# Performance work log

Hardware: AMD Instinct MI355X
Metric: run time of the kernel (lower is better)

## Reference

```python
import jax, jax.numpy as jnp
import numpy as np

B, M, K, E, V, HOPS = 256, 128, 4, 512, 32000, 3


def setup_inputs() -> dict:
    key = jax.random.key(0)
    ks = jax.random.split(key, 12)

    def emb_table(k):
        t = 0.1 * jax.random.normal(k, (V, E), dtype=jnp.float32)
        return t.at[0].set(0.0)  # padding_idx=0

    inp = {
        "context": jax.random.randint(ks[0], (B, M, K), 0, V),
        "y_": jax.random.randint(ks[1], (B,), 0, V),
        "h_": jax.random.normal(ks[2], (1, B, E), dtype=jnp.float32),
        # embedding tables; C[i] tied to A[i+1], so distinct: A0,A1,A2,C2
        "A0": emb_table(ks[3]),
        "A1": emb_table(ks[4]),
        "A2": emb_table(ks[5]),
        "C2": emb_table(ks[6]),
        # GRU (single layer, single step): PyTorch layout [3E, E] and [3E]
        "W_ih": 0.05 * jax.random.normal(ks[7], (3 * E, E), dtype=jnp.float32),
        "W_hh": 0.05 * jax.random.normal(ks[8], (3 * E, E), dtype=jnp.float32),
        "b_ih": jnp.zeros((3 * E,), dtype=jnp.float32),
        "b_hh": jnp.zeros((3 * E,), dtype=jnp.float32),
        # lin_vocab: Linear(2E -> V)
        "lin_W": 0.02 * jax.random.normal(ks[9], (V, 2 * E), dtype=jnp.float32),
        "lin_b": jnp.zeros((V,), dtype=jnp.float32),
    }
    return inp


def _gru_step(x, h, W_ih, W_hh, b_ih, b_hh):
    gi = x @ W_ih.T + b_ih  # [B, 3E]
    gh = h @ W_hh.T + b_hh
    i_r, i_z, i_n = jnp.split(gi, 3, axis=-1)
    h_r, h_z, h_n = jnp.split(gh, 3, axis=-1)
    r = jax.nn.sigmoid(i_r + h_r)
    z = jax.nn.sigmoid(i_z + h_z)
    n = jnp.tanh(i_n + r * h_n)
    return (1.0 - z) * n + z * h


def reference(context, y_, h_, A0, A1, A2, C2, W_ih, W_hh, b_ih, b_hh, lin_W, lin_b):
    # memories[hop] = sum_k A[hop][context], memories[hops] = sum_k C[hops-1][context]
    tables = [A0, A1, A2, C2]
    memories = [t[context].sum(axis=2) for t in tables]  # each [B, M, E]

    m = A1[y_]  # C[0](y_) -- C[0].weight tied to A[1].weight, [B, E]
    h = _gru_step(m, h_[0], W_ih, W_hh, b_ih, b_hh)  # [B, E]

    q = h
    p = None
    p_vocab = None
    for hop in range(HOPS):
        p = jnp.einsum("bme,be->bm", memories[hop], q)  # dot-attention scores
        attn = jax.nn.softmax(p, axis=1)
        o = jnp.einsum("bm,bme->be", attn, memories[hop + 1])
        if hop == 0:
            p_vocab = jnp.concatenate([q, o], axis=1) @ lin_W.T + lin_b  # [B, V]
        q = q + o

    p_ptr = p  # last hop's pre-softmax scores [B, M]
    return (p_ptr, p_vocab, h[None])  # h: [1, B, E]
```

## Files before the change

### kernel.cpp

```cpp
#include <hip/hip_runtime.h>
#include <hip/hip_bf16.h>
#include <stdint.h>
#include <stddef.h>

#define Bb 256
#define Mm 128
#define Ee 512
#define Vv 32000
#define E3 1536

typedef __attribute__((ext_vector_type(8))) short bf16x8;
typedef __attribute__((ext_vector_type(4))) float f32x4;

__device__ __forceinline__ float bf2f(unsigned short u) {
  union { unsigned int i; float f; } v; v.i = ((unsigned int)u) << 16; return v.f;
}
__device__ __forceinline__ unsigned int f2bf(float f) {
  union { float f; unsigned int u; } v; v.f = f;
  unsigned int u = v.u;
  return ((u + 0x7fffu + ((u >> 16) & 1u)) >> 16);
}

#define IN2F_IDX(bb, col)                                                     \
  ((((size_t)((bb) >> 4) * 32 + ((col) >> 5)) * 512) +                        \
   (size_t)((((bb) & 15) + (((col) >> 3) & 3) * 16) * 8 + ((col) & 7)))

__global__ void convert_kernel(const float* __restrict__ A0, const float* __restrict__ A1,
                               const float* __restrict__ A2,
                               unsigned short* __restrict__ tabB) {
  const int t = blockIdx.y;
  const float* src = (t == 0) ? A0 : (t == 1) ? A1 : A2;
  unsigned short* dst = tabB + (size_t)t * Vv * Ee;
  const int n4 = Vv * Ee / 4;
  for (int i = blockIdx.x * blockDim.x + threadIdx.x; i < n4; i += gridDim.x * blockDim.x) {
    f32x4 v = __builtin_nontemporal_load((const f32x4*)src + i);
    unsigned int o0 = f2bf(v.x) | (f2bf(v.y) << 16);
    unsigned int o1 = f2bf(v.z) | (f2bf(v.w) << 16);
    ((uint2*)dst)[i] = make_uint2(o0, o1);
  }
}

__global__ void gru_gemm_kernel(const int* __restrict__ y,
                                const float* __restrict__ A1,
                                const float* __restrict__ hprev,
                                const float* __restrict__ W_ih,
                                const float* __restrict__ W_hh,
                                float* __restrict__ gi,
                                float* __restrict__ gh) {
  const int z = blockIdx.z;
  const float* W = z ? W_hh : W_ih;
  float* C = z ? gh : gi;
  const int by = blockIdx.x * 64;
  const int jy = blockIdx.y * 64;
  __shared__ float As[16][65];
  __shared__ float Bs[16][65];
  const int tx = threadIdx.x & 15, ty = threadIdx.x >> 4;
  float acc[4][4] = {};
  for (int k0 = 0; k0 < Ee; k0 += 16) {
#pragma unroll
    for (int it = 0; it < 4; ++it) {
      int r = ty + it * 16;
      int row = by + r;
      const float* arow = z ? (hprev + (size_t)row * Ee) : (A1 + (size_t)y[row] * Ee);
      As[tx][r] = arow[k0 + tx];
      Bs[tx][r] = W[(size_t)(jy + r) * Ee + k0 + tx];
    }
    __syncthreads();
#pragma unroll
    for (int kk = 0; kk < 16; ++kk) {
      float a[4], bb[4];
#pragma unroll
      for (int i = 0; i < 4; ++i) { a[i] = As[kk][ty * 4 + i]; bb[i] = Bs[kk][tx * 4 + i]; }
#pragma unroll
      for (int i = 0; i < 4; ++i)
#pragma unroll
        for (int j = 0; j < 4; ++j)
          acc[i][j] += a[i] * bb[j];
    }
    __syncthreads();
  }
#pragma unroll
  for (int i = 0; i < 4; ++i)
#pragma unroll
    for (int j = 0; j < 4; ++j)
      C[(size_t)(by + ty * 4 + i) * E3 + jy + tx * 4 + j] = acc[i][j];
}

__global__ __launch_bounds__(1024) void fused_kernel(
    const int* __restrict__ ctx,
    const unsigned short* __restrict__ tabB,
    const float* __restrict__ A0, const float* __restrict__ A1,
    const float* __restrict__ A2,
    const float* __restrict__ gi, const float* __restrict__ gh,
    const float* __restrict__ b_ih, const float* __restrict__ b_hh,
    const float* __restrict__ h0,
    float* __restrict__ out_h, unsigned short* __restrict__ in2f,
    float* __restrict__ p_out) {
  extern __shared__ char smem[];
  unsigned short* Vlds = (unsigned short*)smem;
  float* p_lds = (float*)(smem + 131072);
  float* qbuf = (float*)(smem + 131584);
  float* obuf = (float*)(smem + 133632);

  const int b = blockIdx.x;
  const int tid = threadIdx.x;
  const int lane = tid & 63, w = tid >> 6;

  if (tid < 512) {
    const int e = tid;
    const float* gib = gi + (size_t)b * E3;
    const float* ghb = gh + (size_t)b * E3;
    float ir = gib[e] + b_ih[e];
    float iz = gib[512 + e] + b_ih[512 + e];
    float inn = gib[1024 + e] + b_ih[1024 + e];
    float hr = ghb[e] + b_hh[e];
    float hz = ghb[512 + e] + b_hh[512 + e];
    float hn = ghb[1024 + e] + b_hh[1024 + e];
    float r = 1.f / (1.f + __expf(-(ir + hr)));
    float z = 1.f / (1.f + __expf(-(iz + hz)));
    float n = tanhf(inn + r * hn);
    float hp = h0[(size_t)b * Ee + e];
    float hnew = (1.f - z) * n + z * hp;
    out_h[(size_t)b * Ee + e] = hnew;
    in2f[IN2F_IDX(b, e)] = (unsigned short)f2bf(hnew);
    qbuf[e] = hnew;
  }

#define GATHER_B(T)                                                          \
  {                                                                          \
    const unsigned short* Tb = tabB + (size_t)(T) * ((size_t)Vv * Ee);       \
    _Pragma("unroll 2")                                                      \
    for (int r8 = 0; r8 < 8; ++r8) {                                         \
      const int row = w * 8 + r8;                                            \
      const int4 cc = *(const int4*)(ctx + ((size_t)b * Mm + row) * 4);      \
      uint4 va = *(const uint4*)(Tb + (size_t)cc.x * Ee + lane * 8);         \
      uint4 vb = *(const uint4*)(Tb + (size_t)cc.y * Ee + lane * 8);         \
      uint4 vc = *(const uint4*)(Tb + (size_t)cc.z * Ee + lane * 8);         \
      uint4 vd = *(const uint4*)(Tb + (size_t)cc.w * Ee + lane * 8);         \
      const unsigned int* pa = (const unsigned int*)&va;                     \
      const unsigned int* pb = (const unsigned int*)&vb;                     \
      const unsigned int* pc = (const unsigned int*)&vc;                     \
      const unsigned int* pd = (const unsigned int*)&vd;                     \
      unsigned int o[4];                                                     \
      _Pragma("unroll")                                                      \
      for (int j = 0; j < 4; ++j) {                                          \
        float lo = bf2f((unsigned short)(pa[j] & 0xffff)) +                  \
                   bf2f((unsigned short)(pb[j] & 0xffff)) +                  \
                   bf2f((unsigned short)(pc[j] & 0xffff)) +                  \
                   bf2f((unsigned short)(pd[j] & 0xffff));                   \
        float hi = bf2f((unsigned short)(pa[j] >> 16)) +                     \
                   bf2f((unsigned short)(pb[j] >> 16)) +                     \
                   bf2f((unsigned short)(pc[j] >> 16)) +                     \
                   bf2f((unsigned short)(pd[j] >> 16));                      \
        o[j] = f2bf(lo) | (f2bf(hi) << 16);                                  \
      }                                                                      \
      *(uint4*)(Vlds + (size_t)row * Ee + lane * 8) = *(uint4*)o;            \
    }                                                                        \
  }

#define GATHER_F(TAB)                                                        \
  {                                                                          \
    _Pragma("unroll 2")                                                      \
    for (int r8 = 0; r8 < 8; ++r8) {                                         \
      const int row = w * 8 + r8;                                            \
      const int4 cc = *(const int4*)(ctx + ((size_t)b * Mm + row) * 4);      \
      const float* s0 = TAB + (size_t)cc.x * Ee + lane * 8;                  \
      const float* s1 = TAB + (size_t)cc.y * Ee + lane * 8;                  \
      const float* s2 = TAB + (size_t)cc.z * Ee + lane * 8;                  \
      const float* s3 = TAB + (size_t)cc.w * Ee + lane * 8;                  \
      float4 a0 = *(const float4*)s0, a1 = *(const float4*)(s0 + 4);         \
      float4 b0 = *(const float4*)s1, b1 = *(const float4*)(s1 + 4);         \
      float4 c0 = *(const float4*)s2, c1 = *(const float4*)(s2 + 4);         \
      float4 d0 = *(const float4*)s3, d1 = *(const float4*)(s3 + 4);         \
      unsigned int o[4];                                                     \
      o[0] = f2bf(a0.x + b0.x + c0.x + d0.x) |                               \
             (f2bf(a0.y + b0.y + c0.y + d0.y) << 16);                        \
      o[1] = f2bf(a0.z + b0.z + c0.z + d0.z) |                               \
             (f2bf(a0.w + b0.w + c0.w + d0.w) << 16);                        \
      o[2] = f2bf(a1.x + b1.x + c1.x + d1.x) |                               \
             (f2bf(a1.y + b1.y + c1.y + d1.y) << 16);                        \
      o[3] = f2bf(a1.z + b1.z + c1.z + d1.z) |                               \
             (f2bf(a1.w + b1.w + c1.w + d1.w) << 16);                        \
      *(uint4*)(Vlds + (size_t)row * Ee + lane * 8) = *(uint4*)o;            \
    }                                                                        \
  }

#define GATHER(T, TAB) { if (tabB) GATHER_B(T) else GATHER_F(TAB) }

#define SCORE_PHASE(EMIT)                                                    \
  {                                                                          \
    float qf[8];                                                             \
    *(float4*)&qf[0] = *(const float4*)&qbuf[lane * 8];                      \
    *(float4*)&qf[4] = *(const float4*)&qbuf[lane * 8 + 4];                  \
    _Pragma("unroll")                                                        \
    for (int r = 0; r < 8; ++r) {                                            \
      const int m = w * 8 + r;                                               \
      uint4 kv = *(const uint4*)(Vlds + (size_t)m * Ee + lane * 8);          \
      const unsigned int* p4 = (const unsigned int*)&kv;                     \
      float s = 0.f;                                                         \
      _Pragma("unroll")                                                      \
      for (int x = 0; x < 4; ++x) {                                          \
        s += bf2f((unsigned short)(p4[x] & 0xffff)) * qf[2 * x];             \
        s += bf2f((unsigned short)(p4[x] >> 16)) * qf[2 * x + 1];            \
      }                                                                      \
      _Pragma("unroll")                                                      \
      for (int off = 32; off > 0; off >>= 1) s += __shfl_down(s, off);       \
      if (lane == 0) { EMIT; }                                               \
    }                                                                        \
  }

#define SOFTMAX_PHASE                                                        \
  if (tid < 64) {                                                            \
    float v0 = p_lds[tid], v1 = p_lds[tid + 64];                             \
    float mx = fmaxf(v0, v1);                                                \
    _Pragma("unroll")                                                        \
    for (int off = 32; off > 0; off >>= 1) mx = fmaxf(mx, __shfl_xor(mx, off)); \
    float e0 = __expf(v0 - mx), e1 = __expf(v1 - mx);                        \
    float s = e0 + e1;                                                       \
    _Pragma("unroll")                                                        \
    for (int off = 32; off > 0; off >>= 1) s += __shfl_xor(s, off);          \
    float inv = 1.f / s;                                                     \
    p_lds[tid] = e0 * inv;                                                   \
    p_lds[tid + 64] = e1 * inv;                                              \
  }

#define O_PHASE                                                              \
  {                                                                          \
    const int g = tid >> 8, t = tid & 255;                                   \
    const int e2 = t * 2;                                                    \
    float a0 = 0.f, a1 = 0.f;                                                \
    _Pragma("unroll 4")                                                      \
    for (int m = g * 32; m < g * 32 + 32; ++m) {                             \
      unsigned int vv = *(const unsigned int*)(Vlds + (size_t)m * Ee + e2);  \
      float ww = p_lds[m];                                                   \
      a0 += ww * bf2f((unsigned short)(vv & 0xffff));                        \
      a1 += ww * bf2f((unsigned short)(vv >> 16));                           \
    }                                                                        \
    obuf[g * 512 + e2] = a0;                                                 \
    obuf[g * 512 + e2 + 1] = a1;                                             \
  }

  GATHER(0, A0)
  __syncthreads();
  SCORE_PHASE(p_lds[m] = s)
  __syncthreads();
  SOFTMAX_PHASE
  GATHER(1, A1)
  __syncthreads();
  O_PHASE
  __syncthreads();
  if (tid < 512) {
    const int e = tid;
    float o = obuf[e] + obuf[512 + e] + obuf[1024 + e] + obuf[1536 + e];
    qbuf[e] = qbuf[e] + o;
    in2f[IN2F_IDX(b, 512 + e)] = (unsigned short)f2bf(o);
  }
  __syncthreads();

  SCORE_PHASE(p_lds[m] = s)
  __syncthreads();
  SOFTMAX_PHASE
  GATHER(2, A2)
  __syncthreads();
  O_PHASE
  __syncthreads();
  if (tid < 512) {
    const int e = tid;
    qbuf[e] = qbuf[e] + obuf[e] + obuf[512 + e] + obuf[1024 + e] + obuf[1536 + e];
  }
  __syncthreads();

  SCORE_PHASE(p_out[b * Mm + m] = s)
}

__global__ __launch_bounds__(512) void pvocab_kernel(
    const unsigned short* __restrict__ in2f,
    const float* __restrict__ lin_W,
    const float* __restrict__ lin_b,
    float* __restrict__ out_pv) {
  const int v0 = blockIdx.x * 64;
  const int tid = threadIdx.x;
  const int lane = tid & 63, w = tid >> 6;
  const int wm = w >> 2, wn = w & 3;
  const int l15 = lane & 15, lg = lane >> 4;
  __shared__ __align__(16) unsigned short Ws[2][64][64];

  const int wc = tid & 15, wrb = tid >> 4;

  f32x4 acc[8];
#pragma unroll
  for (int i = 0; i < 8; ++i) acc[i] = (f32x4){0.f, 0.f, 0.f, 0.f};

  float4 wR[2];

#define PV_STAGE_LOAD(K0)                                                    \
  {                                                                          \
    _Pragma("unroll")                                                        \
    for (int it = 0; it < 2; ++it) {                                         \
      int r = wrb + it * 32;                                                 \
      wR[it] = *(const float4*)(lin_W + (size_t)(v0 + r) * 1024 + (K0) + wc * 4); \
    }                                                                        \
  }

#define PV_STAGE_WRITE(BUF)                                                  \
  {                                                                          \
    _Pragma("unroll")                                                        \
    for (int it = 0; it < 2; ++it) {                                         \
      int r = wrb + it * 32;                                                 \
      unsigned int o0 = f2bf(wR[it].x) | (f2bf(wR[it].y) << 16);             \
      unsigned int o1 = f2bf(wR[it].z) | (f2bf(wR[it].w) << 16);             \
      int u = wc >> 1, h = wc & 1;                                           \
      *(uint2*)(&Ws[BUF][r][((u + r) & 7) * 8 + h * 4]) = make_uint2(o0, o1); \
    }                                                                        \
  }

  PV_STAGE_LOAD(0)
  PV_STAGE_WRITE(0)
  __syncthreads();

  int cur = 0;
  for (int t = 0; t < 16; ++t) {
    if (t + 1 < 16) PV_STAGE_LOAD((t + 1) * 64)
#pragma unroll
    for (int kk = 0; kk < 2; ++kk) {
      const int cu = kk * 4 + lg;
      const int kb = t * 2 + kk;
      bf16x8 wf, af[8];
      {
        int row = wn * 16 + l15;
        wf = *(const bf16x8*)(&Ws[cur][row][((cu + row) & 7) * 8]);
      }
#pragma unroll
      for (int i = 0; i < 8; ++i) {
        int mblk = wm * 8 + i;
        af[i] = *(const bf16x8*)(in2f + ((size_t)(mblk * 32 + kb)) * 512 + lane * 8);
      }
#pragma unroll
      for (int i = 0; i < 8; ++i)
        acc[i] = __builtin_amdgcn_mfma_f32_16x16x32_bf16(af[i], wf, acc[i], 0, 0, 0);
    }
    if (t + 1 < 16) {
      PV_STAGE_WRITE(cur ^ 1)
      __syncthreads();
      cur ^= 1;
    }
  }

  {
    int v = v0 + wn * 16 + l15;
    float bias = lin_b[v];
#pragma unroll
    for (int i = 0; i < 8; ++i) {
      int brow = wm * 128 + i * 16 + lg * 4;
#pragma unroll
      for (int rr = 0; rr < 4; ++rr)
        out_pv[(size_t)(brow + rr) * Vv + v] = acc[i][rr] + bias;
    }
  }
}

extern "C" void kernel_launch(void* const* d_in, const int* in_sizes, int n_in,
                              void* d_out, int out_size, void* d_ws, size_t ws_size,
                              hipStream_t stream) {
  const int* ctx = (const int*)d_in[0];
  const int* y = (const int*)d_in[1];
  const float* h0 = (const float*)d_in[2];
  const float* A0 = (const float*)d_in[3];
  const float* A1 = (const float*)d_in[4];
  const float* A2 = (const float*)d_in[5];
  const float* W_ih = (const float*)d_in[7];
  const float* W_hh = (const float*)d_in[8];
  const float* b_ih = (const float*)d_in[9];
  const float* b_hh = (const float*)d_in[10];
  const float* lin_W = (const float*)d_in[11];
  const float* lin_b = (const float*)d_in[12];

  const size_t tabBytes = (size_t)3 * Vv * Ee * 2;
  const size_t giBytes = (size_t)Bb * E3 * 4;
  const size_t in2Bytes = (size_t)Bb * 1024 * 2;
  const bool bf16path = ws_size >= tabBytes + 2 * giBytes + in2Bytes;

  char* ws = (char*)d_ws;
  size_t off = 0;
  unsigned short* tabB = nullptr;
  if (bf16path) { tabB = (unsigned short*)ws; off += tabBytes; }
  float* gi = (float*)(ws + off); off += giBytes;
  float* gh = (float*)(ws + off); off += giBytes;
  unsigned short* in2f = (unsigned short*)(ws + off);

  float* out = (float*)d_out;
  float* p_ptr = out;
  float* p_voc = out + Bb * Mm;
  float* out_h = out + Bb * Mm + (size_t)Bb * Vv;

  if (bf16path)
    convert_kernel<<<dim3(4096, 3), 256, 0, stream>>>(A0, A1, A2, tabB);
  gru_gemm_kernel<<<dim3(4, 24, 2), 256, 0, stream>>>(y, A1, h0, W_ih, W_hh, gi, gh);
  hipFuncSetAttribute((const void*)fused_kernel,
                      hipFuncAttributeMaxDynamicSharedMemorySize, 141824);
  fused_kernel<<<Bb, 1024, 141824, stream>>>(ctx, tabB, A0, A1, A2, gi, gh,
                                             b_ih, b_hh, h0, out_h, in2f, p_ptr);
  pvocab_kernel<<<Vv / 64, 512, 0, stream>>>(in2f, lin_W, lin_b, p_voc);
}
```

Before: 228.7 us.

## Remap pvocab warp tiling and double-buffer A fragments in registers

The p_vocab GEMM kernel changes its per-warp tile from 8 M-blocks × 1 N-fragment to 2 M-blocks × 4 N-fragments. Each warp now loads far fewer A fragments from global memory per k-step and reuses each W fragment from LDS across 2 MFMAs. A fragments are prefetched two iterations ahead into alternating register buffers, and the loop is fully unrolled. The barrier is replaced by an explicit lgkmcnt wait plus s_barrier, and launch bounds request 2 blocks per SM. The costs are higher register pressure and added scheduling complexity.

```diff
diff --git a/kernel.cpp b/kernel.cpp
--- a/kernel.cpp
+++ b/kernel.cpp
@@ -273,36 +273,47 @@
   SCORE_PHASE(p_out[b * Mm + m] = s)
 }
 
-__global__ __launch_bounds__(512) void pvocab_kernel(
+__global__ __launch_bounds__(512, 2) void pvocab_kernel(
     const unsigned short* __restrict__ in2f,
     const float* __restrict__ lin_W,
     const float* __restrict__ lin_b,
     float* __restrict__ out_pv) {
+  __shared__ __align__(16) unsigned short Ws[2][64][64];
+
   const int v0 = blockIdx.x * 64;
   const int tid = threadIdx.x;
   const int lane = tid & 63, w = tid >> 6;
-  const int wm = w >> 2, wn = w & 3;
   const int l15 = lane & 15, lg = lane >> 4;
-  __shared__ __align__(16) unsigned short Ws[2][64][64];
-
   const int wc = tid & 15, wrb = tid >> 4;
 
-  f32x4 acc[8];
-#pragma unroll
-  for (int i = 0; i < 8; ++i) acc[i] = (f32x4){0.f, 0.f, 0.f, 0.f};
-
+  f32x4 acc[2][4];
+#pragma unroll
+  for (int i = 0; i < 2; ++i)
+#pragma unroll
+    for (int j = 0; j < 4; ++j)
+      acc[i][j] = (f32x4){0.f, 0.f, 0.f, 0.f};
+
+  uint4 aA[4], aB[4];
   float4 wR[2];
 
-#define PV_STAGE_LOAD(K0)                                                    \
-  {                                                                          \
-    _Pragma("unroll")                                                        \
-    for (int it = 0; it < 2; ++it) {                                         \
-      int r = wrb + it * 32;                                                 \
-      wR[it] = *(const float4*)(lin_W + (size_t)(v0 + r) * 1024 + (K0) + wc * 4); \
-    }                                                                        \
-  }
-
-#define PV_STAGE_WRITE(BUF)                                                  \
+  const unsigned short* a_base0 = in2f + ((size_t)(2 * w) * 32) * 512 + lane * 8;
+  const unsigned short* a_base1 = in2f + ((size_t)(2 * w + 1) * 32) * 512 + lane * 8;
+
+#define PV_A_LOAD(T, BUF)                                                    \
+  {                                                                          \
+    BUF[0] = *(const uint4*)(a_base0 + (size_t)(2 * (T)) * 512);             \
+    BUF[1] = *(const uint4*)(a_base0 + (size_t)(2 * (T) + 1) * 512);         \
+    BUF[2] = *(const uint4*)(a_base1 + (size_t)(2 * (T)) * 512);             \
+    BUF[3] = *(const uint4*)(a_base1 + (size_t)(2 * (T) + 1) * 512);         \
+  }
+
+#define PV_W_LOAD(T)                                                         \
+  {                                                                          \
+    wR[0] = *(const float4*)(lin_W + (size_t)(v0 + wrb) * 1024 + (T) * 64 + wc * 4);      \
+    wR[1] = *(const float4*)(lin_W + (size_t)(v0 + wrb + 32) * 1024 + (T) * 64 + wc * 4); \
+  }
+
+#define PV_W_WRITE(WWI)                                                      \
   {                                                                          \
     _Pragma("unroll")                                                        \
     for (int it = 0; it < 2; ++it) {                                         \
@@ -310,51 +321,82 @@
       unsigned int o0 = f2bf(wR[it].x) | (f2bf(wR[it].y) << 16);             \
       unsigned int o1 = f2bf(wR[it].z) | (f2bf(wR[it].w) << 16);             \
       int u = wc >> 1, h = wc & 1;                                           \
-      *(uint2*)(&Ws[BUF][r][((u + r) & 7) * 8 + h * 4]) = make_uint2(o0, o1); \
-    }                                                                        \
-  }
-
-  PV_STAGE_LOAD(0)
-  PV_STAGE_WRITE(0)
-  __syncthreads();
-
-  int cur = 0;
-  for (int t = 0; t < 16; ++t) {
-    if (t + 1 < 16) PV_STAGE_LOAD((t + 1) * 64)
-#pragma unroll
-    for (int kk = 0; kk < 2; ++kk) {
-      const int cu = kk * 4 + lg;
-      const int kb = t * 2 + kk;
-      bf16x8 wf, af[8];
-      {
-        int row = wn * 16 + l15;
-        wf = *(const bf16x8*)(&Ws[cur][row][((cu + row) & 7) * 8]);
+      *(uint2*)(&Ws[WWI][r][((u + r) & 7) * 8 + h * 4]) = make_uint2(o0, o1); \
+    }                                                                        \
+  }
+
+#define PV_MFMA(ABUF, RWI)                                                   \
+  {                                                                          \
+    _Pragma("unroll")                                                        \
+    for (int kb = 0; kb < 2; ++kb) {                                         \
+      const int cu = kb * 4 + lg;                                            \
+      bf16x8 wf[4];                                                          \
+      _Pragma("unroll")                                                      \
+      for (int nf = 0; nf < 4; ++nf) {                                       \
+        int row = nf * 16 + l15;                                             \
+        wf[nf] = *(const bf16x8*)(&Ws[RWI][row][((cu + row) & 7) * 8]);      \
+      }                                                                      \
+      _Pragma("unroll")                                                      \
+      for (int mb = 0; mb < 2; ++mb) {                                       \
+        bf16x8 af = *(const bf16x8*)&ABUF[mb * 2 + kb];                      \
+        _Pragma("unroll")                                                    \
+        for (int nf = 0; nf < 4; ++nf)                                       \
+          acc[mb][nf] = __builtin_amdgcn_mfma_f32_16x16x32_bf16(af, wf[nf], acc[mb][nf], 0, 0, 0); \
+      }                                                                      \
+    }                                                                        \
+  }
+
+#define PV_BARRIER                                                           \
+  asm volatile("s_waitcnt lgkmcnt(0)" ::: "memory");                         \
+  __builtin_amdgcn_sched_barrier(0);                                         \
+  __builtin_amdgcn_s_barrier();
+
+#define PV_ITER(T, ABUF, RWI, WWI)                                           \
+  {                                                                          \
+    if ((T) + 1 < 16) PV_W_LOAD((T) + 1)                                     \
+    PV_MFMA(ABUF, RWI)                                                       \
+    if ((T) + 2 < 16) PV_A_LOAD((T) + 2, ABUF)                               \
+    if ((T) + 1 < 16) {                                                      \
+      PV_W_WRITE(WWI)                                                        \
+      PV_BARRIER                                                             \
+    }                                                                        \
+  }
+
+  PV_A_LOAD(0, aA)
+  PV_A_LOAD(1, aB)
+  PV_W_LOAD(0)
+  PV_W_WRITE(0)
+  PV_BARRIER
+
+  PV_ITER(0, aA, 0, 1)
+  PV_ITER(1, aB, 1, 0)
+  PV_ITER(2, aA, 0, 1)
+  PV_ITER(3, aB, 1, 0)
+  PV_ITER(4, aA, 0, 1)
+  PV_ITER(5, aB, 1, 0)
+  PV_ITER(6, aA, 0, 1)
+  PV_ITER(7, aB, 1, 0)
+  PV_ITER(8, aA, 0, 1)
+  PV_ITER(9, aB, 1, 0)
+  PV_ITER(10, aA, 0, 1)
+  PV_ITER(11, aB, 1, 0)
+  PV_ITER(12, aA, 0, 1)
+  PV_ITER(13, aB, 1, 0)
+  PV_ITER(14, aA, 0, 1)
+  PV_ITER(15, aB, 1, 0)
+
+  {
+#pragma unroll
+    for (int nf = 0; nf < 4; ++nf) {
+      int v = v0 + nf * 16 + l15;
+      float bias = lin_b[v];
+#pragma unroll
+      for (int mb = 0; mb < 2; ++mb) {
+        int brow = (2 * w + mb) * 16 + lg * 4;
+#pragma unroll
+        for (int rr = 0; rr < 4; ++rr)
+          out_pv[(size_t)(brow + rr) * Vv + v] = acc[mb][nf][rr] + bias;
       }
-#pragma unroll
-      for (int i = 0; i < 8; ++i) {
-        int mblk = wm * 8 + i;
-        af[i] = *(const bf16x8*)(in2f + ((size_t)(mblk * 32 + kb)) * 512 + lane * 8);
-      }
-#pragma unroll
-      for (int i = 0; i < 8; ++i)
-        acc[i] = __builtin_amdgcn_mfma_f32_16x16x32_bf16(af[i], wf, acc[i], 0, 0, 0);
-    }
-    if (t + 1 < 16) {
-      PV_STAGE_WRITE(cur ^ 1)
-      __syncthreads();
-      cur ^= 1;
-    }
-  }
-
-  {
-    int v = v0 + wn * 16 + l15;
-    float bias = lin_b[v];
-#pragma unroll
-    for (int i = 0; i < 8; ++i) {
-      int brow = wm * 128 + i * 16 + lg * 4;
-#pragma unroll
-      for (int rr = 0; rr < 4; ++rr)
-        out_pv[(size_t)(brow + rr) * Vv + v] = acc[i][rr] + bias;
     }
   }
 }
```

Result: faster. 211.2 us (-7.7%).

## Pipeline lin_W tiles into LDS with async global_load_lds and 5-slot ring

Applied to the files above, without the earlier changes.

Rewrites the p_vocab GEMM kernel so fp32 lin_W tiles are loaded straight into a 5-deep LDS ring with global_load_lds. The loads are issued four steps ahead and waited on with explicit vmcnt waits and barriers. The bf16 conversion moves from the store path to the LDS read path. Each wave now owns two batch row-blocks across all 64 vocab columns instead of an 8x1 tile split, with double-buffered activation fragments prefetched two steps ahead. The goal is to hide global-load latency behind MFMA work and drop the register-staged convert-and-store path, at the cost of doubled LDS footprint (fp32) and a more fragile hand-counted wait schedule.

```diff
diff --git a/kernel.cpp b/kernel.cpp
--- a/kernel.cpp
+++ b/kernel.cpp
@@ -278,83 +278,115 @@
     const float* __restrict__ lin_W,
     const float* __restrict__ lin_b,
     float* __restrict__ out_pv) {
+  __shared__ float Wl[5][2048];
+
   const int v0 = blockIdx.x * 64;
   const int tid = threadIdx.x;
   const int lane = tid & 63, w = tid >> 6;
-  const int wm = w >> 2, wn = w & 3;
   const int l15 = lane & 15, lg = lane >> 4;
-  __shared__ __align__(16) unsigned short Ws[2][64][64];
-
-  const int wc = tid & 15, wrb = tid >> 4;
-
-  f32x4 acc[8];
-#pragma unroll
-  for (int i = 0; i < 8; ++i) acc[i] = (f32x4){0.f, 0.f, 0.f, 0.f};
-
-  float4 wR[2];
-
-#define PV_STAGE_LOAD(K0)                                                    \
+
+  f32x4 acc[2][4];
+#pragma unroll
+  for (int i = 0; i < 2; ++i)
+#pragma unroll
+    for (int j = 0; j < 4; ++j)
+      acc[i][j] = (f32x4){0.f, 0.f, 0.f, 0.f};
+
+  uint4 aA[2], aB[2];
+
+  const unsigned short* a_base0 = in2f + ((size_t)(2 * w) * 32) * 512 + lane * 8;
+  const unsigned short* a_base1 = in2f + ((size_t)(2 * w + 1) * 32) * 512 + lane * 8;
+  const int wrow_l = lane >> 3;
+  const int wc4 = ((lane & 7) ^ (wrow_l & 7)) * 4;
+  const float* wsrc_base = lin_W + (size_t)(v0 + w * 8 + wrow_l) * 1024 + wc4;
+
+#define PV_ISSUE_W(T, SLOT)                                                  \
+  __builtin_amdgcn_global_load_lds(                                          \
+      (const __attribute__((address_space(1))) unsigned int*)(wsrc_base + (T) * 32), \
+      (__attribute__((address_space(3))) unsigned int*)&Wl[SLOT][w * 256],   \
+      16, 0, 0);
+
+#define PV_ISSUE_A(T, BUF)                                                   \
+  BUF[0] = *(const uint4*)(a_base0 + (size_t)(T) * 512);                     \
+  BUF[1] = *(const uint4*)(a_base1 + (size_t)(T) * 512);
+
+#define PV_STEP(T, BUF, RS, WSL, VM)                                         \
+  asm volatile("s_waitcnt vmcnt(" #VM ")\n\ts_barrier" ::: "memory");        \
+  __builtin_amdgcn_sched_barrier(0);                                         \
   {                                                                          \
     _Pragma("unroll")                                                        \
-    for (int it = 0; it < 2; ++it) {                                         \
-      int r = wrb + it * 32;                                                 \
-      wR[it] = *(const float4*)(lin_W + (size_t)(v0 + r) * 1024 + (K0) + wc * 4); \
+    for (int nf = 0; nf < 4; ++nf) {                                         \
+      const int row = nf * 16 + l15;                                         \
+      const int sw = row & 7;                                                \
+      float4 f0 = *(const float4*)&Wl[RS][row * 32 + (((lg * 2) ^ sw) * 4)]; \
+      float4 f1 = *(const float4*)&Wl[RS][row * 32 + ((((lg * 2) + 1) ^ sw) * 4)]; \
+      unsigned int u[4];                                                     \
+      u[0] = f2bf(f0.x) | (f2bf(f0.y) << 16);                                \
+      u[1] = f2bf(f0.z) | (f2bf(f0.w) << 16);                                \
+      u[2] = f2bf(f1.x) | (f2bf(f1.y) << 16);                                \
+      u[3] = f2bf(f1.z) | (f2bf(f1.w) << 16);                                \
+      bf16x8 wf = *(bf16x8*)u;                                               \
+      acc[0][nf] = __builtin_amdgcn_mfma_f32_16x16x32_bf16(                  \
+          *(bf16x8*)&BUF[0], wf, acc[0][nf], 0, 0, 0);                       \
+      acc[1][nf] = __builtin_amdgcn_mfma_f32_16x16x32_bf16(                  \
+          *(bf16x8*)&BUF[1], wf, acc[1][nf], 0, 0, 0);                       \
     }                                                                        \
-  }
-
-#define PV_STAGE_WRITE(BUF)                                                  \
-  {                                                                          \
-    _Pragma("unroll")                                                        \
-    for (int it = 0; it < 2; ++it) {                                         \
-      int r = wrb + it * 32;                                                 \
-      unsigned int o0 = f2bf(wR[it].x) | (f2bf(wR[it].y) << 16);             \
-      unsigned int o1 = f2bf(wR[it].z) | (f2bf(wR[it].w) << 16);             \
-      int u = wc >> 1, h = wc & 1;                                           \
-      *(uint2*)(&Ws[BUF][r][((u + r) & 7) * 8 + h * 4]) = make_uint2(o0, o1); \
-    }                                                                        \
-  }
-
-  PV_STAGE_LOAD(0)
-  PV_STAGE_WRITE(0)
-  __syncthreads();
-
-  int cur = 0;
-  for (int t = 0; t < 16; ++t) {
-    if (t + 1 < 16) PV_STAGE_LOAD((t + 1) * 64)
-#pragma unroll
-    for (int kk = 0; kk < 2; ++kk) {
-      const int cu = kk * 4 + lg;
-      const int kb = t * 2 + kk;
-      bf16x8 wf, af[8];
-      {
-        int row = wn * 16 + l15;
-        wf = *(const bf16x8*)(&Ws[cur][row][((cu + row) & 7) * 8]);
+  }                                                                          \
+  if ((T) + 4 < 32) { PV_ISSUE_W((T) + 4, WSL) }                             \
+  if ((T) + 2 < 32) { PV_ISSUE_A((T) + 2, BUF) }
+
+  PV_ISSUE_W(0, 0)
+  PV_ISSUE_W(1, 1)
+  PV_ISSUE_W(2, 2)
+  PV_ISSUE_A(0, aA)
+  PV_ISSUE_W(3, 3)
+  PV_ISSUE_A(1, aB)
+
+  PV_STEP(0, aA, 0, 4, 3)
+  PV_STEP(1, aB, 1, 0, 3)
+  PV_STEP(2, aA, 2, 1, 3)
+  PV_STEP(3, aB, 3, 2, 3)
+  PV_STEP(4, aA, 4, 3, 3)
+  PV_STEP(5, aB, 0, 4, 3)
+  PV_STEP(6, aA, 1, 0, 3)
+  PV_STEP(7, aB, 2, 1, 3)
+  PV_STEP(8, aA, 3, 2, 3)
+  PV_STEP(9, aB, 4, 3, 3)
+  PV_STEP(10, aA, 0, 4, 3)
+  PV_STEP(11, aB, 1, 0, 3)
+  PV_STEP(12, aA, 2, 1, 3)
+  PV_STEP(13, aB, 3, 2, 3)
+  PV_STEP(14, aA, 4, 3, 3)
+  PV_STEP(15, aB, 0, 4, 3)
+  PV_STEP(16, aA, 1, 0, 3)
+  PV_STEP(17, aB, 2, 1, 3)
+  PV_STEP(18, aA, 3, 2, 3)
+  PV_STEP(19, aB, 4, 3, 3)
+  PV_STEP(20, aA, 0, 4, 3)
+  PV_STEP(21, aB, 1, 0, 3)
+  PV_STEP(22, aA, 2, 1, 3)
+  PV_STEP(23, aB, 3, 2, 3)
+  PV_STEP(24, aA, 4, 3, 3)
+  PV_STEP(25, aB, 0, 4, 3)
+  PV_STEP(26, aA, 1, 0, 3)
+  PV_STEP(27, aB, 2, 1, 3)
+  PV_STEP(28, aA, 3, 2, 3)
+  PV_STEP(29, aB, 4, 3, 2)
+  PV_STEP(30, aA, 0, 4, 2)
+  PV_STEP(31, aB, 1, 0, 0)
+
+  {
+#pragma unroll
+    for (int nf = 0; nf < 4; ++nf) {
+      int v = v0 + nf * 16 + l15;
+      float bias = lin_b[v];
+#pragma unroll
+      for (int mb = 0; mb < 2; ++mb) {
+        int brow = (2 * w + mb) * 16 + lg * 4;
+#pragma unroll
+        for (int rr = 0; rr < 4; ++rr)
+          out_pv[(size_t)(brow + rr) * Vv + v] = acc[mb][nf][rr] + bias;
       }
-#pragma unroll
-      for (int i = 0; i < 8; ++i) {
-        int mblk = wm * 8 + i;
-        af[i] = *(const bf16x8*)(in2f + ((size_t)(mblk * 32 + kb)) * 512 + lane * 8);
-      }
-#pragma unroll
-      for (int i = 0; i < 8; ++i)
-        acc[i] = __builtin_amdgcn_mfma_f32_16x16x32_bf16(af[i], wf, acc[i], 0, 0, 0);
-    }
-    if (t + 1 < 16) {
-      PV_STAGE_WRITE(cur ^ 1)
-      __syncthreads();
-      cur ^= 1;
-    }
-  }
-
-  {
-    int v = v0 + wn * 16 + l15;
-    float bias = lin_b[v];
-#pragma unroll
-    for (int i = 0; i < 8; ++i) {
-      int brow = wm * 128 + i * 16 + lg * 4;
-#pragma unroll
-      for (int rr = 0; rr < 4; ++rr)
-        out_pv[(size_t)(brow + rr) * Vv + v] = acc[i][rr] + bias;
     }
   }
 }
```

New measurement: 217.9 us. 1.05x faster.

## Stage full lin_W tile in LDS and split batch across 16 waves in pvocab

Applied to the files above, without the earlier changes.

The p_vocab GEMM kernel now loads the block's full 64x1024 slice of lin_W into LDS once, converting it to bf16 with an XOR swizzle, instead of streaming it in 64-wide double-buffered K chunks with a barrier per step. The block grows to 1024 threads. Each of the 16 waves owns 16 batch rows and all 64 vocab columns, and prefetches its A fragments in registers with two ping-pong buffers. This removes the per-step barriers and redundant A reloads, but uses 128KB of static LDS per block, which limits occupancy to one block per CU and serializes the weight load before any compute starts.

```diff
diff --git a/kernel.cpp b/kernel.cpp
--- a/kernel.cpp
+++ b/kernel.cpp
@@ -273,88 +273,75 @@
   SCORE_PHASE(p_out[b * Mm + m] = s)
 }
 
-__global__ __launch_bounds__(512) void pvocab_kernel(
+__global__ __launch_bounds__(1024) void pvocab_kernel(
     const unsigned short* __restrict__ in2f,
     const float* __restrict__ lin_W,
     const float* __restrict__ lin_b,
     float* __restrict__ out_pv) {
+  __shared__ __align__(16) unsigned short Ws[64][1024];
+
   const int v0 = blockIdx.x * 64;
   const int tid = threadIdx.x;
   const int lane = tid & 63, w = tid >> 6;
-  const int wm = w >> 2, wn = w & 3;
   const int l15 = lane & 15, lg = lane >> 4;
-  __shared__ __align__(16) unsigned short Ws[2][64][64];
-
-  const int wc = tid & 15, wrb = tid >> 4;
-
-  f32x4 acc[8];
-#pragma unroll
-  for (int i = 0; i < 8; ++i) acc[i] = (f32x4){0.f, 0.f, 0.f, 0.f};
-
-  float4 wR[2];
-
-#define PV_STAGE_LOAD(K0)                                                    \
-  {                                                                          \
+
+  {
+    const float* wsrc = lin_W + (size_t)v0 * 1024;
+#pragma unroll
+    for (int it = 0; it < 16; ++it) {
+      int g = tid + it * 1024;
+      int row = g >> 8;
+      int c4 = g & 255;
+      float4 v = *(const float4*)(wsrc + ((size_t)row * 1024 + c4 * 4));
+      unsigned int o0 = f2bf(v.x) | (f2bf(v.y) << 16);
+      unsigned int o1 = f2bf(v.z) | (f2bf(v.w) << 16);
+      int u = c4 >> 1, h = c4 & 1;
+      int up = u ^ (row & 15);
+      *(uint2*)((char*)&Ws[0][0] + (size_t)row * 2048 + up * 16 + h * 8) =
+          make_uint2(o0, o1);
+    }
+  }
+  __syncthreads();
+
+  f32x4 acc[4];
+#pragma unroll
+  for (int j = 0; j < 4; ++j) acc[j] = (f32x4){0.f, 0.f, 0.f, 0.f};
+
+  const unsigned short* a_base = in2f + ((size_t)w * 32) * 512 + lane * 8;
+
+  uint4 aA = *(const uint4*)(a_base);
+  uint4 aB = *(const uint4*)(a_base + 512);
+
+#define PV_KSTEP(BUF, KB)                                                    \
+  {                                                                          \
+    bf16x8 af = *(bf16x8*)&BUF;                                              \
     _Pragma("unroll")                                                        \
-    for (int it = 0; it < 2; ++it) {                                         \
-      int r = wrb + it * 32;                                                 \
-      wR[it] = *(const float4*)(lin_W + (size_t)(v0 + r) * 1024 + (K0) + wc * 4); \
-    }                                                                        \
-  }
-
-#define PV_STAGE_WRITE(BUF)                                                  \
-  {                                                                          \
-    _Pragma("unroll")                                                        \
-    for (int it = 0; it < 2; ++it) {                                         \
-      int r = wrb + it * 32;                                                 \
-      unsigned int o0 = f2bf(wR[it].x) | (f2bf(wR[it].y) << 16);             \
-      unsigned int o1 = f2bf(wR[it].z) | (f2bf(wR[it].w) << 16);             \
-      int u = wc >> 1, h = wc & 1;                                           \
-      *(uint2*)(&Ws[BUF][r][((u + r) & 7) * 8 + h * 4]) = make_uint2(o0, o1); \
-    }                                                                        \
-  }
-
-  PV_STAGE_LOAD(0)
-  PV_STAGE_WRITE(0)
-  __syncthreads();
-
-  int cur = 0;
-  for (int t = 0; t < 16; ++t) {
-    if (t + 1 < 16) PV_STAGE_LOAD((t + 1) * 64)
-#pragma unroll
-    for (int kk = 0; kk < 2; ++kk) {
-      const int cu = kk * 4 + lg;
-      const int kb = t * 2 + kk;
-      bf16x8 wf, af[8];
-      {
-        int row = wn * 16 + l15;
-        wf = *(const bf16x8*)(&Ws[cur][row][((cu + row) & 7) * 8]);
-      }
-#pragma unroll
-      for (int i = 0; i < 8; ++i) {
-        int mblk = wm * 8 + i;
-        af[i] = *(const bf16x8*)(in2f + ((size_t)(mblk * 32 + kb)) * 512 + lane * 8);
-      }
-#pragma unroll
-      for (int i = 0; i < 8; ++i)
-        acc[i] = __builtin_amdgcn_mfma_f32_16x16x32_bf16(af[i], wf, acc[i], 0, 0, 0);
-    }
-    if (t + 1 < 16) {
-      PV_STAGE_WRITE(cur ^ 1)
-      __syncthreads();
-      cur ^= 1;
-    }
+    for (int nf = 0; nf < 4; ++nf) {                                         \
+      int row = nf * 16 + l15;                                               \
+      int up = ((KB) * 4 + lg) ^ (row & 15);                                 \
+      bf16x8 wf = *(const bf16x8*)((const char*)&Ws[0][0] +                  \
+                                   (size_t)row * 2048 + up * 16);            \
+      acc[nf] = __builtin_amdgcn_mfma_f32_16x16x32_bf16(af, wf, acc[nf], 0, 0, 0); \
+    }                                                                        \
+  }
+
+#pragma unroll
+  for (int kp = 0; kp < 16; ++kp) {
+    PV_KSTEP(aA, 2 * kp)
+    if (kp + 1 < 16) aA = *(const uint4*)(a_base + (size_t)(2 * kp + 2) * 512);
+    PV_KSTEP(aB, 2 * kp + 1)
+    if (kp + 1 < 16) aB = *(const uint4*)(a_base + (size_t)(2 * kp + 3) * 512);
   }
 
   {
-    int v = v0 + wn * 16 + l15;
-    float bias = lin_b[v];
-#pragma unroll
-    for (int i = 0; i < 8; ++i) {
-      int brow = wm * 128 + i * 16 + lg * 4;
+#pragma unroll
+    for (int nf = 0; nf < 4; ++nf) {
+      int v = v0 + nf * 16 + l15;
+      float bias = lin_b[v];
+      int brow = w * 16 + lg * 4;
 #pragma unroll
       for (int rr = 0; rr < 4; ++rr)
-        out_pv[(size_t)(brow + rr) * Vv + v] = acc[i][rr] + bias;
+        out_pv[(size_t)(brow + rr) * Vv + v] = acc[nf][rr] + bias;
     }
   }
 }
@@ -400,5 +387,5 @@
                       hipFuncAttributeMaxDynamicSharedMemorySize, 141824);
   fused_kernel<<<Bb, 1024, 141824, stream>>>(ctx, tabB, A0, A1, A2, gi, gh,
                                              b_ih, b_hh, h0, out_h, in2f, p_ptr);
-  pvocab_kernel<<<Vv / 64, 512, 0, stream>>>(in2f, lin_W, lin_b, p_voc);
-}
+  pvocab_kernel<<<Vv / 64, 1024, 0, stream>>>(in2f, lin_W, lin_b, p_voc);
+}
```

Result: faster. 215.4 us (-5.8%).
